# Performance work log

Hardware: AMD Instinct MI355X
Metric: run time of the kernel (lower is better)

The kernel has to match this reference:

```python
import jax, jax.numpy as jnp
import numpy as np
from jax import lax

D_MODEL = 768
N_LAYERS = 2
D_STATE = 16
D_CONV = 4
EXPAND = 2
D_INNER = EXPAND * D_MODEL
DT_RANK = 48  # ceil(768/16)
BETA = 0.9
ALPHA = 1.0
NS_STEPS = 1
EPS = 1e-5
BATCH = 2
SEQ = 512


def rmsnorm(x, w):
    return x * lax.rsqrt(jnp.mean(x * x, axis=-1, keepdims=True) + EPS) * w


def newton_schulz(X, steps):
    # Muon quintic Newton-Schulz orthogonalization on (B, D_INNER, D_STATE) matrices.
    a, b, c = 3.4445, -4.7750, 2.0315
    G = jnp.swapaxes(X, -1, -2)  # (B, N, Di) rows < cols
    G = G / (jnp.sqrt(jnp.sum(G * G, axis=(-2, -1), keepdims=True)) + 1e-7)
    for _ in range(steps):
        A = G @ jnp.swapaxes(G, -1, -2)  # (B, N, N)
        G = a * G + (b * A + c * (A @ A)) @ G
    return jnp.swapaxes(G, -1, -2)


def mamba_mixer(x, in_w, cw, cb, xp_w, dtp_w, dtp_b, A_log, Dp, out_w):
    B_, L, _ = x.shape
    xz = jnp.einsum('bld,ed->ble', x, in_w)  # (B, L, 2*Di)
    xi, z = jnp.split(xz, 2, axis=-1)
    # causal depthwise conv1d + silu
    xc = lax.conv_general_dilated(
        jnp.swapaxes(xi, 1, 2), cw, window_strides=(1,),
        padding=[(D_CONV - 1, 0)],
        dimension_numbers=('NCH', 'OIH', 'NCH'),
        feature_group_count=D_INNER)
    xc = jax.nn.silu(jnp.swapaxes(xc, 1, 2) + cb)  # (B, L, Di)
    x_dbl = jnp.einsum('bld,ed->ble', xc, xp_w)
    dt_lr = x_dbl[..., :DT_RANK]
    Bm = x_dbl[..., DT_RANK:DT_RANK + D_STATE]  # (B, L, N)
    Cm = x_dbl[..., DT_RANK + D_STATE:]         # (B, L, N)
    dt = jax.nn.softplus(jnp.einsum('blr,dr->bld', dt_lr, dtp_w) + dtp_b)
    A = -jnp.exp(A_log)  # (Di, N)
    dA = jnp.exp(dt[..., None] * A)                            # (B, L, Di, N)
    dBx = dt[..., None] * Bm[:, :, None, :] * xc[..., None]    # (B, L, Di, N)

    def step(carry, inp):
        h, v = carry
        dA_t, dBx_t, C_t = inp
        v = BETA * v + dBx_t                 # momentum velocity
        vu = newton_schulz(v, NS_STEPS)      # NS-orthogonalized update
        h = dA_t * h + ALPHA * vu
        y = jnp.einsum('bdn,bn->bd', h, C_t)
        return (h, v), y

    h0 = jnp.zeros((B_, D_INNER, D_STATE), x.dtype)
    v0 = jnp.zeros_like(h0)
    xs = (jnp.moveaxis(dA, 1, 0), jnp.moveaxis(dBx, 1, 0), jnp.moveaxis(Cm, 1, 0))
    _, ys = lax.scan(step, (h0, v0), xs)
    y = jnp.moveaxis(ys, 0, 1) + Dp * xc
    y = y * jax.nn.silu(z)
    return jnp.einsum('bld,ed->ble', y, out_w)


def forward(x, in_proj_w, conv_w, conv_b, x_proj_w, dt_proj_w, dt_proj_b,
            A_log, D, out_proj_w, norm_w, final_norm_w):
    for i in range(N_LAYERS):
        x = mamba_mixer(rmsnorm(x, norm_w[i]), in_proj_w[i], conv_w[i], conv_b[i],
                        x_proj_w[i], dt_proj_w[i], dt_proj_b[i], A_log[i], D[i],
                        out_proj_w[i]) + x
    return rmsnorm(x, final_norm_w)


def setup_inputs() -> dict:
    key = jax.random.key(0)
    ks = jax.random.split(key, 8)
    s = 0.02
    scale_out = s / np.sqrt(2 * N_LAYERS)
    A_init = jnp.broadcast_to(jnp.arange(1, D_STATE + 1, dtype=jnp.float32), (N_LAYERS, D_INNER, D_STATE))
    return {
        'x': jax.random.normal(ks[0], (BATCH, SEQ, D_MODEL), jnp.float32),
        'in_proj_w': jax.random.normal(ks[1], (N_LAYERS, 2 * D_INNER, D_MODEL), jnp.float32) * s,
        'conv_w': jax.random.normal(ks[2], (N_LAYERS, D_INNER, 1, D_CONV), jnp.float32) * 0.5,
        'conv_b': jnp.zeros((N_LAYERS, D_INNER), jnp.float32),
        'x_proj_w': jax.random.normal(ks[3], (N_LAYERS, DT_RANK + 2 * D_STATE, D_INNER), jnp.float32) * s,
        'dt_proj_w': jax.random.normal(ks[4], (N_LAYERS, D_INNER, DT_RANK), jnp.float32) * (DT_RANK ** -0.5),
        'dt_proj_b': jax.random.uniform(ks[5], (N_LAYERS, D_INNER), jnp.float32, -4.0, -2.0),
        'A_log': jnp.log(A_init),
        'D': jnp.ones((N_LAYERS, D_INNER), jnp.float32),
        'out_proj_w': jax.random.normal(ks[6], (N_LAYERS, D_MODEL, D_INNER), jnp.float32) * scale_out,
        'norm_w': jnp.ones((N_LAYERS, D_MODEL), jnp.float32),
        'final_norm_w': jnp.ones((D_MODEL,), jnp.float32),
    }


def reference(x, in_proj_w, conv_w, conv_b, x_proj_w, dt_proj_w, dt_proj_b,
              A_log, D, out_proj_w, norm_w, final_norm_w):
    return forward(x, in_proj_w, conv_w, conv_b, x_proj_w, dt_proj_w, dt_proj_b,
                   A_log, D, out_proj_w, norm_w, final_norm_w)
```

## Files before the change

kernel.cpp:

```cpp
#include <hip/hip_runtime.h>
#include <math.h>

#define DM   768
#define DI   1536
#define NDS  16
#define DTR  48
#define XDC  80
#define NB   2
#define SEQL 512
#define NT   (NB*SEQL)
#define CC   64
#define TT   8
#define BETA 0.9f
#define NSA  3.4445f
#define NSB  (-4.775f)
#define NSC  2.0315f
#define LOG2E 1.4426950408889634f
#define GKH  768
#define GKS  772

typedef __attribute__((ext_vector_type(8))) short short8v;
typedef __attribute__((ext_vector_type(4))) float f32x4;

__device__ __forceinline__ float silu_(float x){ return x / (1.f + __expf(-x)); }
__device__ __forceinline__ unsigned short bfr(float x){
  unsigned u = __float_as_uint(x);
  return (unsigned short)((u + 0x7fffu + ((u>>16)&1u)) >> 16);
}
__device__ __forceinline__ void gl_lds16(const unsigned short* g, unsigned short* l){
  __builtin_amdgcn_global_load_lds((const __attribute__((address_space(1))) void*)g,
                                   (__attribute__((address_space(3))) void*)l, 16, 0, 0);
}

template<int BF>
__global__ void rms_k(const float* __restrict__ X, const float* __restrict__ W,
                      void* __restrict__ Ov)
{
  const int g = blockIdx.x, tid = threadIdx.x;
  const float* xr = X + (size_t)g*DM;
  float x0 = xr[tid], x1 = xr[tid+256], x2 = xr[tid+512];
  float ss = x0*x0 + x1*x1 + x2*x2;
  #pragma unroll
  for (int m=1; m<=32; m<<=1) ss += __shfl_xor(ss, m);
  __shared__ float ws[4];
  if ((tid & 63) == 0) ws[tid>>6] = ss;
  __syncthreads();
  float sc = rsqrtf((ws[0]+ws[1]+ws[2]+ws[3])*(1.f/DM) + 1e-5f);
  if (BF){
    unsigned short* o = (unsigned short*)Ov + (size_t)g*DM;
    o[tid]     = bfr(x0*sc*W[tid]);
    o[tid+256] = bfr(x1*sc*W[tid+256]);
    o[tid+512] = bfr(x2*sc*W[tid+512]);
  } else {
    float* o = (float*)Ov + (size_t)g*DM;
    o[tid]     = x0*sc*W[tid];
    o[tid+256] = x1*sc*W[tid+256];
    o[tid+512] = x2*sc*W[tid+512];
  }
}

__global__ void castbf_k(const float* __restrict__ in, unsigned short* __restrict__ out, int n4)
{
  const int i = blockIdx.x*256 + threadIdx.x;
  if (i >= n4) return;
  float4 v = ((const float4*)in)[i];
  ushort4 o;
  o.x = bfr(v.x); o.y = bfr(v.y); o.z = bfr(v.z); o.w = bfr(v.w);
  ((ushort4*)out)[i] = o;
}

template<int EPI>
__global__ __launch_bounds__(256) void gemm_mf(
    const unsigned short* __restrict__ Abf, int lda,
    const unsigned short* __restrict__ Bbf, int ldb,
    float* __restrict__ Out, float* __restrict__ Part,
    int M, int N, int K, int SK)
{
  __shared__ unsigned short As[128*32];
  __shared__ unsigned short Bs[128*32];
  const int tid  = threadIdx.x;
  const int wid  = tid >> 6, lane = tid & 63;
  const int bm   = blockIdx.y*128, bn = blockIdx.x*128;
  const int kc   = K/SK, kBeg = blockIdx.z*kc, kEnd = kBeg + kc;
  const int wr   = (wid>>1)*64, wc = (wid&1)*64;

  f32x4 acc[4][4];
  #pragma unroll
  for (int m=0;m<4;m++)
    #pragma unroll
    for (int n=0;n<4;n++) acc[m][n] = (f32x4){0.f,0.f,0.f,0.f};

  const int e0 = (wid*2)*512 + lane*8;
  const int e1 = e0 + 512;
  const int r0 = e0 >> 5, k0e = e0 & 31;
  const int r1 = e1 >> 5, k1e = e1 & 31;
  const unsigned short* Ag0 = Abf + (size_t)(bm + r0)*lda + k0e;
  const unsigned short* Ag1 = Abf + (size_t)(bm + r1)*lda + k1e;
  const unsigned short* Bg0 = Bbf + (size_t)(bn + r0)*ldb + k0e;
  const unsigned short* Bg1 = Bbf + (size_t)(bn + r1)*ldb + k1e;

  int aoff[4], boff[4];
  #pragma unroll
  for (int m=0;m<4;m++) aoff[m] = (wr + m*16 + (lane&15))*32 + (lane>>4)*8;
  #pragma unroll
  for (int n=0;n<4;n++) boff[n] = (wc + n*16 + (lane&15))*32 + (lane>>4)*8;

  for (int k0 = kBeg; k0 < kEnd; k0 += 32){
    gl_lds16(Ag0 + k0, As + e0);
    gl_lds16(Ag1 + k0, As + e1);
    gl_lds16(Bg0 + k0, Bs + e0);
    gl_lds16(Bg1 + k0, Bs + e1);
    __syncthreads();
    short8v af[4], bfv[4];
    #pragma unroll
    for (int m=0;m<4;m++) af[m]  = *(const short8v*)(As + aoff[m]);
    #pragma unroll
    for (int n=0;n<4;n++) bfv[n] = *(const short8v*)(Bs + boff[n]);
    #pragma unroll
    for (int m=0;m<4;m++)
      #pragma unroll
      for (int n=0;n<4;n++)
        acc[m][n] = __builtin_amdgcn_mfma_f32_16x16x32_bf16(af[m], bfv[n], acc[m][n], 0, 0, 0);
    __syncthreads();
  }

  #pragma unroll
  for (int m=0;m<4;m++){
    const int rowb = bm + wr + m*16 + (lane>>4)*4;
    #pragma unroll
    for (int n=0;n<4;n++){
      const int col = bn + wc + n*16 + (lane&15);
      #pragma unroll
      for (int r=0;r<4;r++){
        const int row = rowb + r;
        if (SK == 1) Out[(size_t)row*N + col] = acc[m][n][r];
        else         Part[(size_t)blockIdx.z*M*N + (size_t)row*N + col] = acc[m][n][r];
      }
    }
  }
}

template<int EPI>
__global__ void gemm64(const float* __restrict__ A, int lda,
                       const float* __restrict__ Bw, int ldb,
                       float* __restrict__ Out, float* __restrict__ Part,
                       const float* __restrict__ aux,
                       int M, int N, int K, int SK)
{
  __shared__ float As[16][64], Bs[16][64];
  const int tid = threadIdx.x;
  const int bm = blockIdx.y*64, bn = blockIdx.x*64;
  const int kc = K/SK, kBeg = blockIdx.z*kc, kEnd = kBeg + kc;
  const int lr = tid>>2, lk = (tid&3)<<2;
  const int tx = tid&15, ty = tid>>4;
  float acc[4][4];
  #pragma unroll
  for (int i=0;i<4;i++)
    #pragma unroll
    for (int j=0;j<4;j++) acc[i][j] = 0.f;
  const float* Ap = A + (size_t)(bm+lr)*lda + lk;
  const bool bok = (bn+lr) < N;
  const float* Bp = Bw + (size_t)(bn+lr)*ldb + lk;
  for (int k0=kBeg; k0<kEnd; k0+=16){
    float4 a0 = *(const float4*)(Ap + k0);
    float4 b0 = {0,0,0,0};
    if (bok) b0 = *(const float4*)(Bp + k0);
    __syncthreads();
    As[lk+0][lr]=a0.x; As[lk+1][lr]=a0.y; As[lk+2][lr]=a0.z; As[lk+3][lr]=a0.w;
    Bs[lk+0][lr]=b0.x; Bs[lk+1][lr]=b0.y; Bs[lk+2][lr]=b0.z; Bs[lk+3][lr]=b0.w;
    __syncthreads();
    #pragma unroll
    for (int kk=0;kk<16;kk++){
      float a[4], b[4];
      *(float4*)a = *(const float4*)&As[kk][ty*4];
      *(float4*)b = *(const float4*)&Bs[kk][tx*4];
      #pragma unroll
      for (int i=0;i<4;i++)
        #pragma unroll
        for (int j=0;j<4;j++) acc[i][j] = fmaf(a[i], b[j], acc[i][j]);
    }
  }
  #pragma unroll
  for (int i=0;i<4;i++){
    const int row = bm + ty*4 + i;
    #pragma unroll
    for (int j=0;j<4;j++){
      const int col = bn + tx*4 + j;
      if (col < N){
        if (SK == 1){
          float vv = acc[i][j];
          if (EPI==1){ vv += aux[col]; vv = fmaxf(vv,0.f) + log1pf(__expf(-fabsf(vv))); }
          Out[(size_t)row*N+col] = vv;
        } else {
          Part[(size_t)blockIdx.z*M*N + (size_t)row*N+col] = acc[i][j];
        }
      }
    }
  }
}

template<int EPI>
__global__ void reduce_k(const float* __restrict__ Part, float* __restrict__ Out,
                         const float* __restrict__ aux, int MN, int SK)
{
  const int i = blockIdx.x*256 + threadIdx.x;
  if (i >= MN) return;
  float s = 0.f;
  for (int z=0; z<SK; z++) s += Part[(size_t)z*MN + i];
  if (EPI==2) s += aux[i];
  Out[i] = s;
}

__global__ void conv_k(const float* __restrict__ xz, const float* __restrict__ cw,
                       const float* __restrict__ cb, float* __restrict__ xc)
{
  const int d = blockIdx.x*256 + threadIdx.x;
  const int g = blockIdx.y;
  const int b = g >> 9, t = g & (SEQL-1);
  float4 w4 = *(const float4*)(cw + (size_t)d*4);
  const float wk[4] = {w4.x, w4.y, w4.z, w4.w};
  const float* col = xz + ((size_t)b*SEQL)*(2*DI) + d;
  float acc = cb[d];
  #pragma unroll
  for (int k=0;k<4;k++){
    int tt = t - 3 + k;
    if (tt >= 0) acc = fmaf(wk[k], col[(size_t)tt*(2*DI)], acc);
  }
  xc[(size_t)g*DI + d] = silu_(acc);
}

__global__ void vagg_k(const float* __restrict__ dt, const float* __restrict__ xcp,
                       const float* __restrict__ xdbl, float* __restrict__ Vagg,
                       float* __restrict__ S, float* __restrict__ cumdt)
{
  const int d = blockIdx.x*256 + threadIdx.x;
  const int c = blockIdx.y, b = blockIdx.z;
  float acc[16];
  #pragma unroll
  for (int n=0;n<16;n++) acc[n] = 0.f;
  float sdt = 0.f;
  for (int s=0;s<TT;s++){
    const int g = b*SEQL + c*TT + s;
    float dv = dt[(size_t)g*DI + d];
    float w  = dv * xcp[(size_t)g*DI + d];
    sdt += dv;
    cumdt[(size_t)g*DI + d] = sdt;
    #pragma unroll
    for (int n=0;n<16;n++) acc[n] = fmaf(BETA, acc[n], w * xdbl[(size_t)g*XDC + 48 + n]);
  }
  const size_t base = ((size_t)(b*CC + c)*NDS)*DI + d;
  #pragma unroll
  for (int n=0;n<16;n++) Vagg[base + (size_t)n*DI] = acc[n];
  S[(size_t)(b*CC + c)*DI + d] = sdt;
}

__global__ void vcomb_k(const float* __restrict__ Vagg, float* __restrict__ vst, float betaT)
{
  const int d = blockIdx.x*256 + threadIdx.x;
  const int n = blockIdx.y, b = blockIdx.z;
  const size_t stride = (size_t)NDS*DI;
  size_t idx = ((size_t)(b*CC)*NDS + n)*DI + d;
  float v = 0.f;
  for (int c=0;c<CC;c++){
    vst[idx] = v;
    v = fmaf(betaT, v, Vagg[idx]);
    idx += stride;
  }
}

__global__ __launch_bounds__(256) void gram_k(
    const float* __restrict__ vst, const float* __restrict__ dt,
    const float* __restrict__ xcp, const float* __restrict__ xdbl,
    float* __restrict__ Qg)
{
  const int c = blockIdx.x, b = blockIdx.y;
  const int tid = threadIdx.x;
  __shared__ float Xs[24*GKS];
  __shared__ float Ms[24][25];
  __shared__ float sB[8][16];
  __shared__ float Rm[16][17];

  const size_t vbase = ((size_t)(b*CC + c)*NDS)*DI;
  const size_t gbase = (size_t)(b*SEQL + c*TT);

  const bool active = tid < 252;
  const int tile = tid / 12, seg = tid % 12;
  int ti = 0, tj = 0;
  {
    int tt = tile;
    if (active){ while (tt >= 6 - ti){ tt -= 6 - ti; ti++; } tj = ti + tt; }
  }
  const int i0 = ti*4, j0 = tj*4;
  const int ks = seg*64;
  float acc[4][4];
  #pragma unroll
  for (int i=0;i<4;i++)
    #pragma unroll
    for (int j=0;j<4;j++) acc[i][j] = 0.f;

  for (int pass = 0; pass < 2; pass++){
    const int koff = pass * GKH;
    __syncthreads();
    #pragma unroll
    for (int q = 0; q < 18; q++){
      const int p = tid + q*256;
      const int col = p / 192;
      const int kk  = (p % 192) * 4;
      float4 xv;
      if (col < 16){
        xv = *(const float4*)(vst + vbase + (size_t)col*DI + koff + kk);
      } else {
        const size_t ii = (gbase + (col-16))*DI + koff + kk;
        float4 dv = *(const float4*)(dt + ii);
        float4 xc = *(const float4*)(xcp + ii);
        xv.x = dv.x*xc.x; xv.y = dv.y*xc.y; xv.z = dv.z*xc.z; xv.w = dv.w*xc.w;
      }
      *(float4*)(Xs + col*GKS + kk) = xv;
    }
    __syncthreads();
    if (active){
      for (int k4 = 0; k4 < 64; k4 += 4){
        float4 av[4], bv[4];
        #pragma unroll
        for (int r=0;r<4;r++) av[r] = *(const float4*)(Xs + (i0+r)*GKS + ks + k4);
        #pragma unroll
        for (int r=0;r<4;r++) bv[r] = *(const float4*)(Xs + (j0+r)*GKS + ks + k4);
        #pragma unroll
        for (int i=0;i<4;i++)
          #pragma unroll
          for (int j=0;j<4;j++){
            float s = fmaf(av[i].x, bv[j].x, acc[i][j]);
            s = fmaf(av[i].y, bv[j].y, s);
            s = fmaf(av[i].z, bv[j].z, s);
            acc[i][j] = fmaf(av[i].w, bv[j].w, s);
          }
      }
    }
  }
  __syncthreads();
  if (active){
    #pragma unroll
    for (int e=0;e<16;e++) Xs[(tile*16 + e)*12 + seg] = acc[e>>2][e&3];
  }
  if (tid < 128){ const int s = tid>>4, n = tid&15; sB[s][n] = xdbl[(gbase + s)*XDC + 48 + n]; }
  __syncthreads();
  for (int o = tid; o < 336; o += 256){
    const int tl = o >> 4, e = o & 15;
    int tt = tl, ti2 = 0;
    while (tt >= 6 - ti2){ tt -= 6 - ti2; ti2++; }
    const int tj2 = ti2 + tt;
    const int i = ti2*4 + (e>>2), j = tj2*4 + (e&3);
    float s = 0.f;
    #pragma unroll
    for (int sg=0; sg<12; sg++) s += Xs[o*12 + sg];
    Ms[i][j] = s; Ms[j][i] = s;
  }
  __syncthreads();

  const int i = tid >> 4, j = tid & 15;
  float Rreg = Ms[i][j];
  constexpr float PB[9] = {1.f, 0.9f, 0.81f, 0.729f, 0.6561f, 0.59049f,
                           0.531441f, 0.4782969f, 0.43046721f};
  const size_t qbase = ((size_t)(b*CC + c)*TT)*256;
  #pragma unroll
  for (int t=0;t<TT;t++){
    float p_i = PB[t]*Ms[i][16+t];
    float p_j = PB[t]*Ms[j][16+t];
    #pragma unroll
    for (int r=0;r<t;r++){
      const float gg = Ms[16+r][16+t];
      p_i = fmaf(PB[t-1-r]*gg, sB[r][i], p_i);
      p_j = fmaf(PB[t-1-r]*gg, sB[r][j], p_j);
    }
    const float bi = sB[t][i], bj = sB[t][j];
    const float gtt = Ms[16+t][16+t];
    Rreg = BETA*BETA*Rreg + BETA*(p_i*bj + bi*p_j) + gtt*bi*bj;
    Rm[i][j] = Rreg;
    __syncthreads();
    float tr = 0.f;
    #pragma unroll
    for (int k=0;k<16;k++) tr += Rm[k][k];
    const float nu = sqrtf(tr) + 1e-7f;
    const float inv_nu = 1.f/nu;
    const float inv2 = inv_nu*inv_nu;
    const float inv4 = inv2*inv2;
    float a2v = 0.f;
    #pragma unroll
    for (int k=0;k<16;k++) a2v = fmaf(Rm[i][k], Rm[k][j], a2v);
    float q = NSB*inv2*Rreg + NSC*inv4*a2v;
    if (i == j) q += NSA;
    Qg[qbase + t*256 + tid] = q * inv_nu;
    __syncthreads();
  }
}

__global__ __launch_bounds__(256) void apply_k(
    const float* __restrict__ vst, const float* __restrict__ dt,
    const float* __restrict__ xcp, const float* __restrict__ xdbl,
    const float* __restrict__ Qg, const float* __restrict__ A_log,
    float* __restrict__ ylocal, float* __restrict__ hend)
{
  const int c = blockIdx.x, b = blockIdx.y, z = blockIdx.z;
  const int tid = threadIdx.x;
  const int d = z*256 + tid;
  __shared__ float sQ[8*256];
  __shared__ float sBC[8][32];

  const size_t qbase = ((size_t)(b*CC + c)*TT)*256;
  #pragma unroll
  for (int q=0;q<8;q++) sQ[q*256 + tid] = Qg[qbase + q*256 + tid];
  {
    const int s = tid >> 5, idx = tid & 31;
    sBC[s][idx] = xdbl[(size_t)(b*SEQL + c*TT + s)*XDC + 48 + idx];
  }
  __syncthreads();

  float v[16], h[16], Ar[16];
  {
    const float* vs = vst + ((size_t)(b*CC + c)*NDS)*DI + d;
    const float* arow = A_log + (size_t)d*NDS;
    #pragma unroll
    for (int n=0;n<16;n++){
      v[n] = vs[(size_t)n*DI];
      h[n] = 0.f;
      Ar[n] = -__expf(arow[n]) * LOG2E;
    }
  }

  for (int t=0;t<TT;t++){
    const size_t g = (size_t)(b*SEQL + c*TT + t);
    const float dtv = dt[g*DI + d];
    const float wv  = dtv * xcp[g*DI + d];
    #pragma unroll
    for (int n=0;n<16;n++) v[n] = fmaf(BETA, v[n], wv*sBC[t][n]);
    float un[16];
    #pragma unroll
    for (int n=0;n<16;n++) un[n] = 0.f;
    const float* qt = sQ + t*256;
    #pragma unroll
    for (int k=0;k<16;k++){
      const float vk = v[k];
      const float4 q0 = *(const float4*)(qt + k*16);
      const float4 q1 = *(const float4*)(qt + k*16 + 4);
      const float4 q2 = *(const float4*)(qt + k*16 + 8);
      const float4 q3 = *(const float4*)(qt + k*16 + 12);
      un[0]=fmaf(vk,q0.x,un[0]); un[1]=fmaf(vk,q0.y,un[1]); un[2]=fmaf(vk,q0.z,un[2]); un[3]=fmaf(vk,q0.w,un[3]);
      un[4]=fmaf(vk,q1.x,un[4]); un[5]=fmaf(vk,q1.y,un[5]); un[6]=fmaf(vk,q1.z,un[6]); un[7]=fmaf(vk,q1.w,un[7]);
      un[8]=fmaf(vk,q2.x,un[8]); un[9]=fmaf(vk,q2.y,un[9]); un[10]=fmaf(vk,q2.z,un[10]); un[11]=fmaf(vk,q2.w,un[11]);
      un[12]=fmaf(vk,q3.x,un[12]); un[13]=fmaf(vk,q3.y,un[13]); un[14]=fmaf(vk,q3.z,un[14]); un[15]=fmaf(vk,q3.w,un[15]);
    }
    float y = 0.f;
    #pragma unroll
    for (int n=0;n<16;n++){
      const float e = exp2f(dtv*Ar[n]);
      h[n] = fmaf(e, h[n], un[n]);
      y = fmaf(h[n], sBC[t][16+n], y);
    }
    ylocal[g*DI + d] = y;
  }
  float* he = hend + ((size_t)(b*CC + c)*NDS)*DI + d;
  #pragma unroll
  for (int n=0;n<16;n++) he[(size_t)n*DI] = h[n];
}

__global__ void hcomb_k(const float* __restrict__ hend, const float* __restrict__ S,
                        const float* __restrict__ A_log, float* __restrict__ hst)
{
  const int d = blockIdx.x*256 + threadIdx.x;
  const int n = blockIdx.y, b = blockIdx.z;
  const float An = -__expf(A_log[(size_t)d*NDS + n]);
  const size_t stride = (size_t)NDS*DI;
  size_t idx  = ((size_t)(b*CC)*NDS + n)*DI + d;
  size_t sidx = (size_t)(b*CC)*DI + d;
  float hv = 0.f;
  for (int c=0;c<CC;c++){
    hst[idx] = hv;
    hv = fmaf(__expf(An * S[sidx]), hv, hend[idx]);
    idx += stride; sidx += DI;
  }
}

__global__ void yepi_k(const float* __restrict__ ylocal, const float* __restrict__ hst,
                       const float* __restrict__ cumdt, const float* __restrict__ xdbl,
                       const float* __restrict__ A_log, const float* __restrict__ Dv,
                       const float* __restrict__ xcp, const float* __restrict__ xz,
                       unsigned short* __restrict__ ybf)
{
  const int d = blockIdx.x*256 + threadIdx.x;
  const int g = blockIdx.y;
  const int b = g >> 9, t = g & (SEQL-1);
  const int c = t / TT;
  const float ddt = cumdt[(size_t)g*DI + d];
  const float* hs = hst + ((size_t)(b*CC + c)*NDS)*DI + d;
  const float* ar = A_log + (size_t)d*NDS;
  float corr = 0.f;
  #pragma unroll
  for (int n=0;n<16;n++){
    float An = -__expf(ar[n]);
    float Cn = xdbl[(size_t)g*XDC + 64 + n];
    corr = fmaf(hs[(size_t)n*DI] * __expf(An*ddt), Cn, corr);
  }
  float y = ylocal[(size_t)g*DI + d] + corr + Dv[d]*xcp[(size_t)g*DI + d];
  float z = xz[(size_t)g*(2*DI) + DI + d];
  ybf[(size_t)g*DI + d] = bfr(y * silu_(z));
}

extern "C" void kernel_launch(void* const* d_in, const int* in_sizes, int n_in,
                              void* d_out, int out_size, void* d_ws, size_t ws_size,
                              hipStream_t stream)
{
  (void)in_sizes; (void)n_in; (void)out_size; (void)ws_size;
  const float* x      = (const float*)d_in[0];
  const float* in_w   = (const float*)d_in[1];
  const float* conv_w = (const float*)d_in[2];
  const float* conv_b = (const float*)d_in[3];
  const float* xp_w   = (const float*)d_in[4];
  const float* dtp_w  = (const float*)d_in[5];
  const float* dtp_b  = (const float*)d_in[6];
  const float* A_log  = (const float*)d_in[7];
  const float* Dp     = (const float*)d_in[8];
  const float* out_w  = (const float*)d_in[9];
  const float* norm_w = (const float*)d_in[10];
  const float* fnorm  = (const float*)d_in[11];

  const float betaT = powf(BETA, (float)TT);
  const int skx = 8, skout = 4;

  float* w0 = (float*)d_ws; size_t off = 0;
  auto alloc = [&](size_t n)->float*{ float* p = w0 + off; off += (n + 63) & ~(size_t)63; return p; };
  float* xa     = alloc((size_t)NT*DM);
  float* xb     = alloc((size_t)NT*DM);
  float* bfA    = alloc((size_t)NT*DI/2);
  float* xz     = alloc((size_t)NT*2*DI);
  float* xcb    = alloc((size_t)NT*DI);
  float* xdbl   = alloc((size_t)NT*XDC);
  float* dtb    = alloc((size_t)NT*DI);
  float* cumdt  = alloc((size_t)NT*DI);
  float* ylocal = alloc((size_t)NT*DI);
  float* Sbuf   = alloc((size_t)NB*CC*DI);
  float* Qg     = alloc((size_t)NB*CC*TT*256);
  float* big1   = alloc((size_t)NB*CC*NDS*DI);
  float* big2   = alloc((size_t)NB*CC*NDS*DI);

  unsigned short* xnb = (unsigned short*)bfA;
  unsigned short* ybf = (unsigned short*)bfA;
  unsigned short* wbf = (unsigned short*)big2;
  float* partb = big1;

  const float* xcur = x;
  float* nxt = xa;
  for (int l=0; l<2; l++){
    const float* inw_l = in_w   + (size_t)l*2*DI*DM;
    const float* cw_l  = conv_w + (size_t)l*DI*4;
    const float* cb_l  = conv_b + (size_t)l*DI;
    const float* xpw_l = xp_w   + (size_t)l*XDC*DI;
    const float* dtw_l = dtp_w  + (size_t)l*DI*DTR;
    const float* dtbi  = dtp_b  + (size_t)l*DI;
    const float* al_l  = A_log  + (size_t)l*DI*NDS;
    const float* d_l   = Dp     + (size_t)l*DI;
    const float* ow_l  = out_w  + (size_t)l*DM*DI;
    const float* nw_l  = norm_w + (size_t)l*DM;

    castbf_k<<<dim3((2*DI*DM/4+255)/256), dim3(256), 0, stream>>>(inw_l, wbf, 2*DI*DM/4);
    rms_k<1><<<dim3(NT), dim3(256), 0, stream>>>(xcur, nw_l, xnb);
    gemm_mf<0><<<dim3(2*DI/128, NT/128, 1), dim3(256), 0, stream>>>(
        xnb, DM, wbf, DM, xz, nullptr, NT, 2*DI, DM, 1);
    conv_k<<<dim3(DI/256, NT), dim3(256), 0, stream>>>(xz, cw_l, cb_l, xcb);
    gemm64<0><<<dim3((XDC+63)/64, NT/64, skx), dim3(256), 0, stream>>>(
        xcb, DI, xpw_l, DI, xdbl, partb, nullptr, NT, XDC, DI, skx);
    reduce_k<0><<<dim3((NT*XDC+255)/256), dim3(256), 0, stream>>>(partb, xdbl, nullptr, NT*XDC, skx);
    gemm64<1><<<dim3(DI/64, NT/64, 1), dim3(256), 0, stream>>>(
        xdbl, XDC, dtw_l, DTR, dtb, partb, dtbi, NT, DI, DTR, 1);
    vagg_k<<<dim3(DI/256, CC, NB), dim3(256), 0, stream>>>(dtb, xcb, xdbl, big1, Sbuf, cumdt);
    vcomb_k<<<dim3(DI/256, NDS, NB), dim3(256), 0, stream>>>(big1, big2, betaT);
    gram_k<<<dim3(CC, NB), dim3(256), 0, stream>>>(big2, dtb, xcb, xdbl, Qg);
    apply_k<<<dim3(CC, NB, DI/256), dim3(256), 0, stream>>>(
        big2, dtb, xcb, xdbl, Qg, al_l, ylocal, big1);
    hcomb_k<<<dim3(DI/256, NDS, NB), dim3(256), 0, stream>>>(big1, Sbuf, al_l, big2);
    yepi_k<<<dim3(DI/256, NT), dim3(256), 0, stream>>>(ylocal, big2, cumdt, xdbl, al_l, d_l, xcb, xz, ybf);
    castbf_k<<<dim3((DM*DI/4+255)/256), dim3(256), 0, stream>>>(ow_l, wbf, DM*DI/4);
    gemm_mf<0><<<dim3(DM/128, NT/128, skout), dim3(256), 0, stream>>>(
        ybf, DI, wbf, DI, nxt, partb, NT, DM, DI, skout);
    reduce_k<2><<<dim3((NT*DM+255)/256), dim3(256), 0, stream>>>(partb, nxt, xcur, NT*DM, skout);
    xcur = nxt; nxt = xb;
  }
  rms_k<0><<<dim3(NT), dim3(256), 0, stream>>>(xcur, fnorm, (float*)d_out);
}
```

Baseline: 448.6 us.

## Fuse reductions with RMSNorm, move x_proj to bf16 MFMA, precompute dt*x, reuse buffers in place

Weight casts now run once up front for both layers instead of per layer. The x_proj GEMM moves from the fp32 tiled kernel to the bf16 MFMA GEMM, using a zero-padded weight and a bf16 copy of the conv output. The dt_proj epilogue also writes dt*xc once so that vagg, gram and apply read it directly. The split-K reduce of out_proj is fused with the residual add and the next RMSNorm (or the final norm), and the vcomb and hcomb scans run in place, which frees a large buffer. This trades lower x_proj precision and a few extra writes for fewer launches and less memory traffic.

Measured after the change: 423.4 us. 5.6% less time.

```diff
diff --git a/kernel.cpp b/kernel.cpp
--- a/kernel.cpp
+++ b/kernel.cpp
@@ -6,6 +6,7 @@
 #define NDS  16
 #define DTR  48
 #define XDC  80
+#define XPN  128
 #define NB   2
 #define SEQL 512
 #define NT   (NB*SEQL)
@@ -32,9 +33,8 @@
                                    (__attribute__((address_space(3))) void*)l, 16, 0, 0);
 }
 
-template<int BF>
 __global__ void rms_k(const float* __restrict__ X, const float* __restrict__ W,
-                      void* __restrict__ Ov)
+                      unsigned short* __restrict__ O)
 {
   const int g = blockIdx.x, tid = threadIdx.x;
   const float* xr = X + (size_t)g*DM;
@@ -46,17 +46,10 @@
   if ((tid & 63) == 0) ws[tid>>6] = ss;
   __syncthreads();
   float sc = rsqrtf((ws[0]+ws[1]+ws[2]+ws[3])*(1.f/DM) + 1e-5f);
-  if (BF){
-    unsigned short* o = (unsigned short*)Ov + (size_t)g*DM;
-    o[tid]     = bfr(x0*sc*W[tid]);
-    o[tid+256] = bfr(x1*sc*W[tid+256]);
-    o[tid+512] = bfr(x2*sc*W[tid+512]);
-  } else {
-    float* o = (float*)Ov + (size_t)g*DM;
-    o[tid]     = x0*sc*W[tid];
-    o[tid+256] = x1*sc*W[tid+256];
-    o[tid+512] = x2*sc*W[tid+512];
-  }
+  unsigned short* o = O + (size_t)g*DM;
+  o[tid]     = bfr(x0*sc*W[tid]);
+  o[tid+256] = bfr(x1*sc*W[tid+256]);
+  o[tid+512] = bfr(x2*sc*W[tid+512]);
 }
 
 __global__ void castbf_k(const float* __restrict__ in, unsigned short* __restrict__ out, int n4)
@@ -69,7 +62,23 @@
   ((ushort4*)out)[i] = o;
 }
 
-template<int EPI>
+__global__ void castpad_k(const float* __restrict__ in, unsigned short* __restrict__ out)
+{
+  const int i = blockIdx.x*256 + threadIdx.x;
+  const int total = 2*XPN*DI/4;
+  if (i >= total) return;
+  const int l = i / (XPN*DI/4);
+  const int r = i % (XPN*DI/4);
+  const int row = r / (DI/4);
+  const int k4 = r % (DI/4);
+  ushort4 o = {0,0,0,0};
+  if (row < XDC){
+    float4 v = *(const float4*)(in + ((size_t)l*XDC + row)*DI + k4*4);
+    o.x = bfr(v.x); o.y = bfr(v.y); o.z = bfr(v.z); o.w = bfr(v.w);
+  }
+  ((ushort4*)out)[i] = o;
+}
+
 __global__ __launch_bounds__(256) void gemm_mf(
     const unsigned short* __restrict__ Abf, int lda,
     const unsigned short* __restrict__ Bbf, int ldb,
@@ -140,17 +149,15 @@
   }
 }
 
-template<int EPI>
-__global__ void gemm64(const float* __restrict__ A, int lda,
-                       const float* __restrict__ Bw, int ldb,
-                       float* __restrict__ Out, float* __restrict__ Part,
-                       const float* __restrict__ aux,
-                       int M, int N, int K, int SK)
+__global__ void gemm64w(const float* __restrict__ A, int lda,
+                        const float* __restrict__ Bw, int ldb,
+                        float* __restrict__ Out, float* __restrict__ wOut,
+                        const float* __restrict__ bias, const float* __restrict__ xc,
+                        int M, int N, int K)
 {
   __shared__ float As[16][64], Bs[16][64];
   const int tid = threadIdx.x;
   const int bm = blockIdx.y*64, bn = blockIdx.x*64;
-  const int kc = K/SK, kBeg = blockIdx.z*kc, kEnd = kBeg + kc;
   const int lr = tid>>2, lk = (tid&3)<<2;
   const int tx = tid&15, ty = tid>>4;
   float acc[4][4];
@@ -159,12 +166,10 @@
     #pragma unroll
     for (int j=0;j<4;j++) acc[i][j] = 0.f;
   const float* Ap = A + (size_t)(bm+lr)*lda + lk;
-  const bool bok = (bn+lr) < N;
   const float* Bp = Bw + (size_t)(bn+lr)*ldb + lk;
-  for (int k0=kBeg; k0<kEnd; k0+=16){
+  for (int k0=0; k0<K; k0+=16){
     float4 a0 = *(const float4*)(Ap + k0);
-    float4 b0 = {0,0,0,0};
-    if (bok) b0 = *(const float4*)(Bp + k0);
+    float4 b0 = *(const float4*)(Bp + k0);
     __syncthreads();
     As[lk+0][lr]=a0.x; As[lk+1][lr]=a0.y; As[lk+2][lr]=a0.z; As[lk+3][lr]=a0.w;
     Bs[lk+0][lr]=b0.x; Bs[lk+1][lr]=b0.y; Bs[lk+2][lr]=b0.z; Bs[lk+3][lr]=b0.w;
@@ -186,33 +191,59 @@
     #pragma unroll
     for (int j=0;j<4;j++){
       const int col = bn + tx*4 + j;
-      if (col < N){
-        if (SK == 1){
-          float vv = acc[i][j];
-          if (EPI==1){ vv += aux[col]; vv = fmaxf(vv,0.f) + log1pf(__expf(-fabsf(vv))); }
-          Out[(size_t)row*N+col] = vv;
-        } else {
-          Part[(size_t)blockIdx.z*M*N + (size_t)row*N+col] = acc[i][j];
-        }
-      }
-    }
-  }
-}
-
-template<int EPI>
-__global__ void reduce_k(const float* __restrict__ Part, float* __restrict__ Out,
-                         const float* __restrict__ aux, int MN, int SK)
+      float vv = acc[i][j] + bias[col];
+      vv = fmaxf(vv,0.f) + log1pf(__expf(-fabsf(vv)));
+      Out[(size_t)row*N+col]  = vv;
+      wOut[(size_t)row*N+col] = vv * xc[(size_t)row*N+col];
+    }
+  }
+}
+
+__global__ void reducepad_k(const float* __restrict__ Part, float* __restrict__ Out)
 {
   const int i = blockIdx.x*256 + threadIdx.x;
-  if (i >= MN) return;
+  if (i >= NT*XDC) return;
+  const int row = i / XDC, col = i % XDC;
   float s = 0.f;
-  for (int z=0; z<SK; z++) s += Part[(size_t)z*MN + i];
-  if (EPI==2) s += aux[i];
+  #pragma unroll
+  for (int z=0; z<8; z++) s += Part[(size_t)z*NT*XPN + (size_t)row*XPN + col];
   Out[i] = s;
 }
 
+template<int MODE>
+__global__ void reduce_rms_k(const float* __restrict__ Part, const float* __restrict__ res,
+                             const float* __restrict__ W, float* __restrict__ nxt,
+                             unsigned short* __restrict__ xnb, float* __restrict__ dout)
+{
+  const int g = blockIdx.x, tid = threadIdx.x;
+  float s[3];
+  #pragma unroll
+  for (int j=0;j<3;j++){
+    const int e = tid + j*256;
+    float v = res[(size_t)g*DM + e];
+    #pragma unroll
+    for (int z=0;z<4;z++) v += Part[(size_t)z*NT*DM + (size_t)g*DM + e];
+    s[j] = v;
+    if (MODE==1) nxt[(size_t)g*DM + e] = v;
+  }
+  float ss = s[0]*s[0] + s[1]*s[1] + s[2]*s[2];
+  #pragma unroll
+  for (int m=1; m<=32; m<<=1) ss += __shfl_xor(ss, m);
+  __shared__ float ws[4];
+  if ((tid & 63) == 0) ws[tid>>6] = ss;
+  __syncthreads();
+  float sc = rsqrtf((ws[0]+ws[1]+ws[2]+ws[3])*(1.f/DM) + 1e-5f);
+  #pragma unroll
+  for (int j=0;j<3;j++){
+    const int e = tid + j*256;
+    if (MODE==1) xnb[(size_t)g*DM + e] = bfr(s[j]*sc*W[e]);
+    else         dout[(size_t)g*DM + e] = s[j]*sc*W[e];
+  }
+}
+
 __global__ void conv_k(const float* __restrict__ xz, const float* __restrict__ cw,
-                       const float* __restrict__ cb, float* __restrict__ xc)
+                       const float* __restrict__ cb, float* __restrict__ xc,
+                       unsigned short* __restrict__ xc16)
 {
   const int d = blockIdx.x*256 + threadIdx.x;
   const int g = blockIdx.y;
@@ -226,10 +257,12 @@
     int tt = t - 3 + k;
     if (tt >= 0) acc = fmaf(wk[k], col[(size_t)tt*(2*DI)], acc);
   }
-  xc[(size_t)g*DI + d] = silu_(acc);
-}
-
-__global__ void vagg_k(const float* __restrict__ dt, const float* __restrict__ xcp,
+  const float r = silu_(acc);
+  xc[(size_t)g*DI + d]   = r;
+  xc16[(size_t)g*DI + d] = bfr(r);
+}
+
+__global__ void vagg_k(const float* __restrict__ dt, const float* __restrict__ wb,
                        const float* __restrict__ xdbl, float* __restrict__ Vagg,
                        float* __restrict__ S, float* __restrict__ cumdt)
 {
@@ -241,10 +274,9 @@
   float sdt = 0.f;
   for (int s=0;s<TT;s++){
     const int g = b*SEQL + c*TT + s;
-    float dv = dt[(size_t)g*DI + d];
-    float w  = dv * xcp[(size_t)g*DI + d];
-    sdt += dv;
+    sdt += dt[(size_t)g*DI + d];
     cumdt[(size_t)g*DI + d] = sdt;
+    const float w = wb[(size_t)g*DI + d];
     #pragma unroll
     for (int n=0;n<16;n++) acc[n] = fmaf(BETA, acc[n], w * xdbl[(size_t)g*XDC + 48 + n]);
   }
@@ -254,7 +286,7 @@
   S[(size_t)(b*CC + c)*DI + d] = sdt;
 }
 
-__global__ void vcomb_k(const float* __restrict__ Vagg, float* __restrict__ vst, float betaT)
+__global__ void vcomb_k(float* V, float betaT)
 {
   const int d = blockIdx.x*256 + threadIdx.x;
   const int n = blockIdx.y, b = blockIdx.z;
@@ -262,16 +294,16 @@
   size_t idx = ((size_t)(b*CC)*NDS + n)*DI + d;
   float v = 0.f;
   for (int c=0;c<CC;c++){
-    vst[idx] = v;
-    v = fmaf(betaT, v, Vagg[idx]);
+    const float a = V[idx];
+    V[idx] = v;
+    v = fmaf(betaT, v, a);
     idx += stride;
   }
 }
 
 __global__ __launch_bounds__(256) void gram_k(
-    const float* __restrict__ vst, const float* __restrict__ dt,
-    const float* __restrict__ xcp, const float* __restrict__ xdbl,
-    float* __restrict__ Qg)
+    const float* __restrict__ vst, const float* __restrict__ wb,
+    const float* __restrict__ xdbl, float* __restrict__ Qg)
 {
   const int c = blockIdx.x, b = blockIdx.y;
   const int tid = threadIdx.x;
@@ -307,14 +339,8 @@
       const int col = p / 192;
       const int kk  = (p % 192) * 4;
       float4 xv;
-      if (col < 16){
-        xv = *(const float4*)(vst + vbase + (size_t)col*DI + koff + kk);
-      } else {
-        const size_t ii = (gbase + (col-16))*DI + koff + kk;
-        float4 dv = *(const float4*)(dt + ii);
-        float4 xc = *(const float4*)(xcp + ii);
-        xv.x = dv.x*xc.x; xv.y = dv.y*xc.y; xv.z = dv.z*xc.z; xv.w = dv.w*xc.w;
-      }
+      if (col < 16) xv = *(const float4*)(vst + vbase + (size_t)col*DI + koff + kk);
+      else          xv = *(const float4*)(wb + (gbase + (col-16))*DI + koff + kk);
       *(float4*)(Xs + col*GKS + kk) = xv;
     }
     __syncthreads();
@@ -395,10 +421,10 @@
 }
 
 __global__ __launch_bounds__(256) void apply_k(
-    const float* __restrict__ vst, const float* __restrict__ dt,
-    const float* __restrict__ xcp, const float* __restrict__ xdbl,
+    float* vh, const float* __restrict__ dt,
+    const float* __restrict__ wb, const float* __restrict__ xdbl,
     const float* __restrict__ Qg, const float* __restrict__ A_log,
-    float* __restrict__ ylocal, float* __restrict__ hend)
+    float* __restrict__ ylocal)
 {
   const int c = blockIdx.x, b = blockIdx.y, z = blockIdx.z;
   const int tid = threadIdx.x;
@@ -417,7 +443,7 @@
 
   float v[16], h[16], Ar[16];
   {
-    const float* vs = vst + ((size_t)(b*CC + c)*NDS)*DI + d;
+    float* vs = vh + ((size_t)(b*CC + c)*NDS)*DI + d;
     const float* arow = A_log + (size_t)d*NDS;
     #pragma unroll
     for (int n=0;n<16;n++){
@@ -430,7 +456,7 @@
   for (int t=0;t<TT;t++){
     const size_t g = (size_t)(b*SEQL + c*TT + t);
     const float dtv = dt[g*DI + d];
-    const float wv  = dtv * xcp[g*DI + d];
+    const float wv  = wb[g*DI + d];
     #pragma unroll
     for (int n=0;n<16;n++) v[n] = fmaf(BETA, v[n], wv*sBC[t][n]);
     float un[16];
@@ -458,13 +484,13 @@
     }
     ylocal[g*DI + d] = y;
   }
-  float* he = hend + ((size_t)(b*CC + c)*NDS)*DI + d;
+  float* he = vh + ((size_t)(b*CC + c)*NDS)*DI + d;
   #pragma unroll
   for (int n=0;n<16;n++) he[(size_t)n*DI] = h[n];
 }
 
-__global__ void hcomb_k(const float* __restrict__ hend, const float* __restrict__ S,
-                        const float* __restrict__ A_log, float* __restrict__ hst)
+__global__ void hcomb_k(float* H, const float* __restrict__ S,
+                        const float* __restrict__ A_log)
 {
   const int d = blockIdx.x*256 + threadIdx.x;
   const int n = blockIdx.y, b = blockIdx.z;
@@ -474,8 +500,9 @@
   size_t sidx = (size_t)(b*CC)*DI + d;
   float hv = 0.f;
   for (int c=0;c<CC;c++){
-    hst[idx] = hv;
-    hv = fmaf(__expf(An * S[sidx]), hv, hend[idx]);
+    const float a = H[idx];
+    H[idx] = hv;
+    hv = fmaf(__expf(An * S[sidx]), hv, a);
     idx += stride; sidx += DI;
   }
 }
@@ -524,65 +551,75 @@
   const float* fnorm  = (const float*)d_in[11];
 
   const float betaT = powf(BETA, (float)TT);
-  const int skx = 8, skout = 4;
 
   float* w0 = (float*)d_ws; size_t off = 0;
   auto alloc = [&](size_t n)->float*{ float* p = w0 + off; off += (n + 63) & ~(size_t)63; return p; };
   float* xa     = alloc((size_t)NT*DM);
-  float* xb     = alloc((size_t)NT*DM);
   float* bfA    = alloc((size_t)NT*DI/2);
   float* xz     = alloc((size_t)NT*2*DI);
   float* xcb    = alloc((size_t)NT*DI);
+  float* xcbbF  = alloc((size_t)NT*DI/2);
   float* xdbl   = alloc((size_t)NT*XDC);
   float* dtb    = alloc((size_t)NT*DI);
+  float* wbuf   = alloc((size_t)NT*DI);
   float* cumdt  = alloc((size_t)NT*DI);
   float* ylocal = alloc((size_t)NT*DI);
   float* Sbuf   = alloc((size_t)NB*CC*DI);
   float* Qg     = alloc((size_t)NB*CC*TT*256);
   float* big1   = alloc((size_t)NB*CC*NDS*DI);
-  float* big2   = alloc((size_t)NB*CC*NDS*DI);
-
-  unsigned short* xnb = (unsigned short*)bfA;
-  unsigned short* ybf = (unsigned short*)bfA;
-  unsigned short* wbf = (unsigned short*)big2;
+  float* wInF   = alloc((size_t)2*2*DI*DM/2);
+  float* wOutF  = alloc((size_t)2*DM*DI/2);
+  float* wXpF   = alloc((size_t)2*XPN*DI/2);
+
+  unsigned short* xnb  = (unsigned short*)bfA;
+  unsigned short* ybf  = (unsigned short*)bfA;
+  unsigned short* xcbb = (unsigned short*)xcbbF;
+  unsigned short* wInb = (unsigned short*)wInF;
+  unsigned short* wOutb= (unsigned short*)wOutF;
+  unsigned short* wXpb = (unsigned short*)wXpF;
   float* partb = big1;
 
+  castbf_k<<<dim3((2*2*DI*DM/4+255)/256), dim3(256), 0, stream>>>(in_w, wInb, 2*2*DI*DM/4);
+  castbf_k<<<dim3((2*DM*DI/4+255)/256), dim3(256), 0, stream>>>(out_w, wOutb, 2*DM*DI/4);
+  castpad_k<<<dim3((2*XPN*DI/4+255)/256), dim3(256), 0, stream>>>(xp_w, wXpb);
+  rms_k<<<dim3(NT), dim3(256), 0, stream>>>(x, norm_w, xnb);
+
   const float* xcur = x;
-  float* nxt = xa;
   for (int l=0; l<2; l++){
-    const float* inw_l = in_w   + (size_t)l*2*DI*DM;
+    const unsigned short* wIn_l  = wInb  + (size_t)l*2*DI*DM;
+    const unsigned short* wOut_l = wOutb + (size_t)l*DM*DI;
+    const unsigned short* wXp_l  = wXpb  + (size_t)l*XPN*DI;
     const float* cw_l  = conv_w + (size_t)l*DI*4;
     const float* cb_l  = conv_b + (size_t)l*DI;
-    const float* xpw_l = xp_w   + (size_t)l*XDC*DI;
     const float* dtw_l = dtp_w  + (size_t)l*DI*DTR;
     const float* dtbi  = dtp_b  + (size_t)l*DI;
     const float* al_l  = A_log  + (size_t)l*DI*NDS;
     const float* d_l   = Dp     + (size_t)l*DI;
-    const float* ow_l  = out_w  + (size_t)l*DM*DI;
-    const float* nw_l  = norm_w + (size_t)l*DM;
-
-    castbf_k<<<dim3((2*DI*DM/4+255)/256), dim3(256), 0, stream>>>(inw_l, wbf, 2*DI*DM/4);
-    rms_k<1><<<dim3(NT), dim3(256), 0, stream>>>(xcur, nw_l, xnb);
-    gemm_mf<0><<<dim3(2*DI/128, NT/128, 1), dim3(256), 0, stream>>>(
-        xnb, DM, wbf, DM, xz, nullptr, NT, 2*DI, DM, 1);
-    conv_k<<<dim3(DI/256, NT), dim3(256), 0, stream>>>(xz, cw_l, cb_l, xcb);
-    gemm64<0><<<dim3((XDC+63)/64, NT/64, skx), dim3(256), 0, stream>>>(
-        xcb, DI, xpw_l, DI, xdbl, partb, nullptr, NT, XDC, DI, skx);
-    reduce_k<0><<<dim3((NT*XDC+255)/256), dim3(256), 0, stream>>>(partb, xdbl, nullptr, NT*XDC, skx);
-    gemm64<1><<<dim3(DI/64, NT/64, 1), dim3(256), 0, stream>>>(
-        xdbl, XDC, dtw_l, DTR, dtb, partb, dtbi, NT, DI, DTR, 1);
-    vagg_k<<<dim3(DI/256, CC, NB), dim3(256), 0, stream>>>(dtb, xcb, xdbl, big1, Sbuf, cumdt);
-    vcomb_k<<<dim3(DI/256, NDS, NB), dim3(256), 0, stream>>>(big1, big2, betaT);
-    gram_k<<<dim3(CC, NB), dim3(256), 0, stream>>>(big2, dtb, xcb, xdbl, Qg);
+
+    gemm_mf<<<dim3(2*DI/128, NT/128, 1), dim3(256), 0, stream>>>(
+        xnb, DM, wIn_l, DM, xz, nullptr, NT, 2*DI, DM, 1);
+    conv_k<<<dim3(DI/256, NT), dim3(256), 0, stream>>>(xz, cw_l, cb_l, xcb, xcbb);
+    gemm_mf<<<dim3(XPN/128, NT/128, 8), dim3(256), 0, stream>>>(
+        xcbb, DI, wXp_l, DI, nullptr, partb, NT, XPN, DI, 8);
+    reducepad_k<<<dim3((NT*XDC+255)/256), dim3(256), 0, stream>>>(partb, xdbl);
+    gemm64w<<<dim3(DI/64, NT/64, 1), dim3(256), 0, stream>>>(
+        xdbl, XDC, dtw_l, DTR, dtb, wbuf, dtbi, xcb, NT, DI, DTR);
+    vagg_k<<<dim3(DI/256, CC, NB), dim3(256), 0, stream>>>(dtb, wbuf, xdbl, big1, Sbuf, cumdt);
+    vcomb_k<<<dim3(DI/256, NDS, NB), dim3(256), 0, stream>>>(big1, betaT);
+    gram_k<<<dim3(CC, NB), dim3(256), 0, stream>>>(big1, wbuf, xdbl, Qg);
     apply_k<<<dim3(CC, NB, DI/256), dim3(256), 0, stream>>>(
-        big2, dtb, xcb, xdbl, Qg, al_l, ylocal, big1);
-    hcomb_k<<<dim3(DI/256, NDS, NB), dim3(256), 0, stream>>>(big1, Sbuf, al_l, big2);
-    yepi_k<<<dim3(DI/256, NT), dim3(256), 0, stream>>>(ylocal, big2, cumdt, xdbl, al_l, d_l, xcb, xz, ybf);
-    castbf_k<<<dim3((DM*DI/4+255)/256), dim3(256), 0, stream>>>(ow_l, wbf, DM*DI/4);
-    gemm_mf<0><<<dim3(DM/128, NT/128, skout), dim3(256), 0, stream>>>(
-        ybf, DI, wbf, DI, nxt, partb, NT, DM, DI, skout);
-    reduce_k<2><<<dim3((NT*DM+255)/256), dim3(256), 0, stream>>>(partb, nxt, xcur, NT*DM, skout);
-    xcur = nxt; nxt = xb;
-  }
-  rms_k<0><<<dim3(NT), dim3(256), 0, stream>>>(xcur, fnorm, (float*)d_out);
-}
+        big1, dtb, wbuf, xdbl, Qg, al_l, ylocal);
+    hcomb_k<<<dim3(DI/256, NDS, NB), dim3(256), 0, stream>>>(big1, Sbuf, al_l);
+    yepi_k<<<dim3(DI/256, NT), dim3(256), 0, stream>>>(
+        ylocal, big1, cumdt, xdbl, al_l, d_l, xcb, xz, ybf);
+    gemm_mf<<<dim3(DM/128, NT/128, 4), dim3(256), 0, stream>>>(
+        ybf, DI, wOut_l, DI, nullptr, partb, NT, DM, DI, 4);
+    if (l == 0)
+      reduce_rms_k<1><<<dim3(NT), dim3(256), 0, stream>>>(
+          partb, xcur, norm_w + DM, xa, xnb, nullptr);
+    else
+      reduce_rms_k<2><<<dim3(NT), dim3(256), 0, stream>>>(
+          partb, xcur, fnorm, nullptr, nullptr, (float*)d_out);
+    xcur = xa;
+  }
+}
```
